# Kernel optimization log

Hardware: AMD Instinct MI355X
Metric: run time of the kernel (lower is better)

## Reference

```python
import jax, jax.numpy as jnp
import numpy as np

N_QUBITS = 4
N_LAYERS = 2
DIM = 2 ** N_QUBITS  # 16
B = 262144


def _cnot_perm(c, t):
    # wire 0 is the most significant bit (pennylane default.qubit convention)
    idx = np.arange(DIM)
    cb = (idx >> (N_QUBITS - 1 - c)) & 1
    return idx ^ (cb << (N_QUBITS - 1 - t))

# all-pairs CNOTs (i, j) for i < j, applied once per layer
CNOT_PERMS = [jnp.asarray(_cnot_perm(i, j)) for i in range(N_QUBITS) for j in range(i + 1, N_QUBITS)]


def _rx(t):
    c = jnp.cos(t / 2).astype(jnp.complex64)
    s = jnp.sin(t / 2).astype(jnp.complex64)
    return jnp.stack([jnp.stack([c, -1j * s], -1), jnp.stack([-1j * s, c], -1)], -2)


def _ry(t):
    c = jnp.cos(t / 2).astype(jnp.complex64)
    s = jnp.sin(t / 2).astype(jnp.complex64)
    return jnp.stack([jnp.stack([c, -s], -1), jnp.stack([s, c], -1)], -2)


def _rz(t):
    e = jnp.exp(-1j * t.astype(jnp.complex64) / 2)
    z = jnp.zeros_like(e)
    return jnp.stack([jnp.stack([e, z], -1), jnp.stack([z, jnp.conj(e)], -1)], -2)


def _apply_1q(state, gate, wire):
    # state: [B, 2,2,2,2]; gate: [2,2] (shared) or [B,2,2] (per-sample)
    ax = 1 + wire
    s = jnp.moveaxis(state, ax, -1)
    if gate.ndim == 2:
        s = jnp.einsum('b...i,ji->b...j', s, gate)
    else:
        s = jnp.einsum('b...i,bji->b...j', s, gate)
    return jnp.moveaxis(s, -1, ax)


def _circuit(x, qw):
    # x: [B, 4] rotation angles; qw: [24] circuit weights. Returns <Z_0>: [B]
    b = x.shape[0]
    state = jnp.zeros((b, DIM), jnp.complex64).at[:, 0].set(1.0)
    state = state.reshape((b,) + (2,) * N_QUBITS)
    for i in range(N_QUBITS):
        state = _apply_1q(state, _rx(x[:, i]), i)
        state = _apply_1q(state, _rz(x[:, i]), i)
    for layer in range(N_LAYERS):
        for i in range(N_QUBITS):
            state = _apply_1q(state, _ry(qw[layer * N_QUBITS + i]), i)
            state = _apply_1q(state, _rz(qw[layer * N_QUBITS + i + N_QUBITS]), i)
        flat = state.reshape(b, DIM)
        for p in CNOT_PERMS:
            flat = flat[:, p]
        state = flat.reshape((b,) + (2,) * N_QUBITS)
        for i in range(N_QUBITS):
            state = _apply_1q(state, _rx(qw[layer * N_QUBITS + i + 2 * N_QUBITS]), i)
    probs = jnp.abs(state.reshape(b, DIM)) ** 2
    zvec = jnp.where(jnp.arange(DIM) < DIM // 2, 1.0, -1.0).astype(probs.dtype)
    return probs @ zvec


def _mlp(q, W1, b1, W2, b2, W3, b3, W4, b4):
    h = jax.nn.relu(q @ W1.T + b1)
    h = jax.nn.relu(h @ W2.T + b2)
    h = jax.nn.relu(h @ W3.T + b3)
    return jax.nn.sigmoid(h @ W4.T + b4)


def setup_inputs() -> dict:
    key = jax.random.key(0)
    ks = jax.random.split(key, 10)
    def lin(k, fo, fi):
        bound = 1.0 / np.sqrt(fi)
        k1, k2 = jax.random.split(k)
        return (jax.random.uniform(k1, (fo, fi), jnp.float32, -bound, bound),
                jax.random.uniform(k2, (fo,), jnp.float32, -bound, bound))
    W1, b1 = lin(ks[2], 32, 1)
    W2, b2 = lin(ks[3], 16, 32)
    W3, b3 = lin(ks[4], 8, 16)
    W4, b4 = lin(ks[5], 1, 8)
    return {
        'x': jax.random.normal(ks[0], (B, N_QUBITS), jnp.float32),
        'qw': jax.random.normal(ks[1], (N_LAYERS * N_QUBITS * 3,), jnp.float32),
        'W1': W1, 'b1': b1, 'W2': W2, 'b2': b2,
        'W3': W3, 'b3': b3, 'W4': W4, 'b4': b4,
    }


def reference(x, qw, W1, b1, W2, b2, W3, b3, W4, b4):
    q = _circuit(x, qw)[:, None]  # [B, 1] quantum expectation values
    return _mlp(q, W1, b1, W2, b2, W3, b3, W4, b4)
```

## Files before the change

### kernel.cpp

```cpp
#include <hip/hip_runtime.h>
#include <math.h>

#define DIM 16

__device__ __forceinline__ void cmul(float ar, float ai, float br, float bi,
                                     float& cr, float& ci) {
  cr = ar * br - ai * bi;
  ci = ar * bi + ai * br;
}

template <int TB>
__device__ __forceinline__ void apply_ryrz(float (&sr)[DIM], float (&si)[DIM],
                                           float cy, float sy, float cz, float sz) {
#pragma unroll
  for (int i = 0; i < DIM; ++i) {
    if (i & TB) continue;
    const int j = i | TB;
    float a0r = sr[i], a0i = si[i], a1r = sr[j], a1i = si[j];
    float t0r = cy * a0r - sy * a1r;
    float t0i = cy * a0i - sy * a1i;
    float t1r = sy * a0r + cy * a1r;
    float t1i = sy * a0i + cy * a1i;
    sr[i] = cz * t0r + sz * t0i;
    si[i] = cz * t0i - sz * t0r;
    sr[j] = cz * t1r - sz * t1i;
    si[j] = cz * t1i + sz * t1r;
  }
}

template <int TB>
__device__ __forceinline__ void apply_rx(float (&sr)[DIM], float (&si)[DIM],
                                         float cx, float sx) {
#pragma unroll
  for (int i = 0; i < DIM; ++i) {
    if (i & TB) continue;
    const int j = i | TB;
    float a0r = sr[i], a0i = si[i], a1r = sr[j], a1i = si[j];
    sr[i] = cx * a0r + sx * a1i;
    si[i] = cx * a0i - sx * a1r;
    sr[j] = cx * a1r + sx * a0i;
    si[j] = cx * a1i - sx * a0r;
  }
}

template <int CB, int TB>
__device__ __forceinline__ void apply_cnot(float (&sr)[DIM], float (&si)[DIM]) {
#pragma unroll
  for (int i = 0; i < DIM; ++i) {
    if (!(i & CB)) continue;
    if (i & TB) continue;
    const int j = i | TB;
    float tr = sr[i], ti = si[i];
    sr[i] = sr[j]; si[i] = si[j];
    sr[j] = tr;    si[j] = ti;
  }
}

__global__ __launch_bounds__(256) void qnn_kernel(
    const float* __restrict__ x, const float* __restrict__ qw,
    const float* __restrict__ W1, const float* __restrict__ b1,
    const float* __restrict__ W2, const float* __restrict__ b2,
    const float* __restrict__ W3, const float* __restrict__ b3,
    const float* __restrict__ W4, const float* __restrict__ b4,
    float* __restrict__ out, int B) {
  int b = blockIdx.x * blockDim.x + threadIdx.x;
  if (b >= B) return;

  float4 xv = reinterpret_cast<const float4*>(x)[b];
  float xs[4] = {xv.x, xv.y, xv.z, xv.w};

  float ur[4][2], ui[4][2];
#pragma unroll
  for (int i = 0; i < 4; ++i) {
    float s, c;
    __sincosf(0.5f * xs[i], &s, &c);
    ur[i][0] = c * c;
    ur[i][1] = s * s;
    ui[i][0] = -c * s;
    ui[i][1] = -c * s;
  }

  float a01r[4], a01i[4], a23r[4], a23i[4];
#pragma unroll
  for (int i0 = 0; i0 < 2; ++i0)
#pragma unroll
    for (int i1 = 0; i1 < 2; ++i1) {
      cmul(ur[0][i0], ui[0][i0], ur[1][i1], ui[1][i1], a01r[i0 * 2 + i1], a01i[i0 * 2 + i1]);
      cmul(ur[2][i0], ui[2][i0], ur[3][i1], ui[3][i1], a23r[i0 * 2 + i1], a23i[i0 * 2 + i1]);
    }
  float sr[DIM], si[DIM];
#pragma unroll
  for (int i = 0; i < DIM; ++i)
    cmul(a01r[i >> 2], a01i[i >> 2], a23r[i & 3], a23i[i & 3], sr[i], si[i]);

#pragma unroll
  for (int layer = 0; layer < 2; ++layer) {
    const int o = layer * 4;

#define RYRZ_W(WIRE, TB)                                                     \
  {                                                                          \
    float sy, cy, sz, cz;                                                    \
    __sincosf(0.5f * qw[o + WIRE], &sy, &cy);                                \
    __sincosf(0.5f * qw[o + WIRE + 4], &sz, &cz);                            \
    apply_ryrz<TB>(sr, si, cy, sy, cz, sz);                                  \
  }
    RYRZ_W(0, 8)
    RYRZ_W(1, 4)
    RYRZ_W(2, 2)
    RYRZ_W(3, 1)
#undef RYRZ_W

    apply_cnot<8, 4>(sr, si);
    apply_cnot<8, 2>(sr, si);
    apply_cnot<8, 1>(sr, si);
    apply_cnot<4, 2>(sr, si);
    apply_cnot<4, 1>(sr, si);
    apply_cnot<2, 1>(sr, si);

#define RX_W(WIRE, TB)                                                       \
  {                                                                          \
    float sx, cx;                                                            \
    __sincosf(0.5f * qw[o + WIRE + 8], &sx, &cx);                            \
    apply_rx<TB>(sr, si, cx, sx);                                            \
  }
    RX_W(0, 8)
    RX_W(1, 4)
    RX_W(2, 2)
    RX_W(3, 1)
#undef RX_W
  }

  float q = 0.f;
#pragma unroll
  for (int i = 0; i < DIM; ++i) {
    float p = fmaf(sr[i], sr[i], si[i] * si[i]);
    q += (i < 8) ? p : -p;
  }

  float h1[32];
#pragma unroll
  for (int j = 0; j < 32; ++j) h1[j] = fmaxf(0.f, fmaf(q, W1[j], b1[j]));

  float h2[16];
#pragma unroll
  for (int k = 0; k < 16; ++k) {
    float acc = b2[k];
#pragma unroll
    for (int j = 0; j < 32; ++j) acc = fmaf(W2[k * 32 + j], h1[j], acc);
    h2[k] = fmaxf(0.f, acc);
  }

  float h3[8];
#pragma unroll
  for (int k = 0; k < 8; ++k) {
    float acc = b3[k];
#pragma unroll
    for (int j = 0; j < 16; ++j) acc = fmaf(W3[k * 16 + j], h2[j], acc);
    h3[k] = fmaxf(0.f, acc);
  }

  float acc = b4[0];
#pragma unroll
  for (int j = 0; j < 8; ++j) acc = fmaf(W4[j], h3[j], acc);

  out[b] = 1.f / (1.f + __expf(-acc));
}

extern "C" void kernel_launch(void* const* d_in, const int* in_sizes, int n_in,
                              void* d_out, int out_size, void* d_ws, size_t ws_size,
                              hipStream_t stream) {
  const float* x  = (const float*)d_in[0];
  const float* qw = (const float*)d_in[1];
  const float* W1 = (const float*)d_in[2];
  const float* b1 = (const float*)d_in[3];
  const float* W2 = (const float*)d_in[4];
  const float* b2 = (const float*)d_in[5];
  const float* W3 = (const float*)d_in[6];
  const float* b3 = (const float*)d_in[7];
  const float* W4 = (const float*)d_in[8];
  const float* b4 = (const float*)d_in[9];
  float* out = (float*)d_out;

  const int B = in_sizes[0] / 4;
  const int block = 256;
  const int grid = (B + block - 1) / block;
  qnn_kernel<<<grid, block, 0, stream>>>(x, qw, W1, b1, W2, b2, W3, b3, W4, b4,
                                         out, B);
}
```

Measured before the change: 89.88 us.

## Fold first-layer rotations into product state and fuse middle gates via setup kernel

Adds a tiny setup kernel that computes the weight-dependent trig values once and writes them to the workspace. Because single-qubit gates commute past nothing but are still local before the first CNOT block, the first layer's Ry/Rz are folded into the per-wire product-state construction. Layer 0's Rx and layer 1's Ry and Rz are merged into one 2x2 unitary per wire. This cuts the number of full 16-amplitude gate sweeps and removes per-thread sincos on uniform weights, at the cost of an extra kernel launch and dense complex 2x2 multiplies.

```diff
diff --git a/kernel.cpp b/kernel.cpp
--- a/kernel.cpp
+++ b/kernel.cpp
@@ -2,6 +2,38 @@
 #include <math.h>
 
 #define DIM 16
+
+__global__ void qnn_setup(const float* __restrict__ qw, float* __restrict__ ws) {
+  int w = threadIdx.x;
+  if (w >= 4) return;
+  float a = qw[0 + w];
+  float b = qw[4 + w];
+  float e0 = qw[8 + w];
+  float c = qw[4 + w];
+  float d = qw[8 + w];
+  float e1 = qw[12 + w];
+
+  ws[w * 4 + 0] = cosf(0.5f * a);
+  ws[w * 4 + 1] = sinf(0.5f * a);
+  ws[w * 4 + 2] = cosf(0.5f * b);
+  ws[w * 4 + 3] = sinf(0.5f * b);
+
+  float cc = cosf(0.5f * c), sc = sinf(0.5f * c);
+  float ce = cosf(0.5f * e0), se = sinf(0.5f * e0);
+  float m00r = cc * ce, m00i =  sc * se;
+  float m01r = -sc * ce, m01i = -cc * se;
+  float m10r =  sc * ce, m10i = -cc * se;
+  float m11r =  cc * ce, m11i = -sc * se;
+  float cd = cosf(0.5f * d), sd = sinf(0.5f * d);
+  float* u = ws + 16 + w * 8;
+  u[0] = cd * m00r + sd * m00i;  u[1] = cd * m00i - sd * m00r;
+  u[2] = cd * m01r + sd * m01i;  u[3] = cd * m01i - sd * m01r;
+  u[4] = cd * m10r - sd * m10i;  u[5] = cd * m10i + sd * m10r;
+  u[6] = cd * m11r - sd * m11i;  u[7] = cd * m11i + sd * m11r;
+
+  ws[48 + w * 2 + 0] = cosf(0.5f * e1);
+  ws[48 + w * 2 + 1] = sinf(0.5f * e1);
+}
 
 __device__ __forceinline__ void cmul(float ar, float ai, float br, float bi,
                                      float& cr, float& ci) {
@@ -10,21 +42,19 @@
 }
 
 template <int TB>
-__device__ __forceinline__ void apply_ryrz(float (&sr)[DIM], float (&si)[DIM],
-                                           float cy, float sy, float cz, float sz) {
+__device__ __forceinline__ void apply_u(float (&sr)[DIM], float (&si)[DIM],
+                                        float u00r, float u00i, float u01r, float u01i,
+                                        float u10r, float u10i, float u11r, float u11i) {
 #pragma unroll
   for (int i = 0; i < DIM; ++i) {
     if (i & TB) continue;
     const int j = i | TB;
-    float a0r = sr[i], a0i = si[i], a1r = sr[j], a1i = si[j];
-    float t0r = cy * a0r - sy * a1r;
-    float t0i = cy * a0i - sy * a1i;
-    float t1r = sy * a0r + cy * a1r;
-    float t1i = sy * a0i + cy * a1i;
-    sr[i] = cz * t0r + sz * t0i;
-    si[i] = cz * t0i - sz * t0r;
-    sr[j] = cz * t1r - sz * t1i;
-    si[j] = cz * t1i + sz * t1r;
+    float ar = sr[i], ai = si[i], br = sr[j], bi = si[j];
+    float nr = u00r * ar - u00i * ai + u01r * br - u01i * bi;
+    float ni = u00r * ai + u00i * ar + u01r * bi + u01i * br;
+    float mr = u10r * ar - u10i * ai + u11r * br - u11i * bi;
+    float mi = u10r * ai + u10i * ar + u11r * bi + u11i * br;
+    sr[i] = nr; si[i] = ni; sr[j] = mr; si[j] = mi;
   }
 }
 
@@ -57,7 +87,7 @@
 }
 
 __global__ __launch_bounds__(256) void qnn_kernel(
-    const float* __restrict__ x, const float* __restrict__ qw,
+    const float* __restrict__ x, const float* __restrict__ ws,
     const float* __restrict__ W1, const float* __restrict__ b1,
     const float* __restrict__ W2, const float* __restrict__ b2,
     const float* __restrict__ W3, const float* __restrict__ b3,
@@ -71,13 +101,17 @@
 
   float ur[4][2], ui[4][2];
 #pragma unroll
-  for (int i = 0; i < 4; ++i) {
+  for (int w = 0; w < 4; ++w) {
     float s, c;
-    __sincosf(0.5f * xs[i], &s, &c);
-    ur[i][0] = c * c;
-    ur[i][1] = s * s;
-    ui[i][0] = -c * s;
-    ui[i][1] = -c * s;
+    __sincosf(0.5f * xs[w], &s, &c);
+    float v0r0 = c * c, v0i0 = -c * s;
+    float v0r1 = s * s, v0i1 = -c * s;
+    float cy = ws[w * 4 + 0], sy = ws[w * 4 + 1];
+    float cz = ws[w * 4 + 2], sz = ws[w * 4 + 3];
+    float t0r = cy * v0r0 - sy * v0r1, t0i = cy * v0i0 - sy * v0i1;
+    float t1r = sy * v0r0 + cy * v0r1, t1i = sy * v0i0 + cy * v0i1;
+    ur[w][0] = cz * t0r + sz * t0i;  ui[w][0] = cz * t0i - sz * t0r;
+    ur[w][1] = cz * t1r - sz * t1i;  ui[w][1] = cz * t1i + sz * t1r;
   }
 
   float a01r[4], a01i[4], a23r[4], a23i[4];
@@ -93,42 +127,35 @@
   for (int i = 0; i < DIM; ++i)
     cmul(a01r[i >> 2], a01i[i >> 2], a23r[i & 3], a23i[i & 3], sr[i], si[i]);
 
-#pragma unroll
-  for (int layer = 0; layer < 2; ++layer) {
-    const int o = layer * 4;
-
-#define RYRZ_W(WIRE, TB)                                                     \
-  {                                                                          \
-    float sy, cy, sz, cz;                                                    \
-    __sincosf(0.5f * qw[o + WIRE], &sy, &cy);                                \
-    __sincosf(0.5f * qw[o + WIRE + 4], &sz, &cz);                            \
-    apply_ryrz<TB>(sr, si, cy, sy, cz, sz);                                  \
-  }
-    RYRZ_W(0, 8)
-    RYRZ_W(1, 4)
-    RYRZ_W(2, 2)
-    RYRZ_W(3, 1)
-#undef RYRZ_W
-
-    apply_cnot<8, 4>(sr, si);
-    apply_cnot<8, 2>(sr, si);
-    apply_cnot<8, 1>(sr, si);
-    apply_cnot<4, 2>(sr, si);
-    apply_cnot<4, 1>(sr, si);
-    apply_cnot<2, 1>(sr, si);
-
-#define RX_W(WIRE, TB)                                                       \
-  {                                                                          \
-    float sx, cx;                                                            \
-    __sincosf(0.5f * qw[o + WIRE + 8], &sx, &cx);                            \
-    apply_rx<TB>(sr, si, cx, sx);                                            \
-  }
-    RX_W(0, 8)
-    RX_W(1, 4)
-    RX_W(2, 2)
-    RX_W(3, 1)
-#undef RX_W
-  }
+  apply_cnot<8, 4>(sr, si);
+  apply_cnot<8, 2>(sr, si);
+  apply_cnot<8, 1>(sr, si);
+  apply_cnot<4, 2>(sr, si);
+  apply_cnot<4, 1>(sr, si);
+  apply_cnot<2, 1>(sr, si);
+
+#define APPLY_U(WIRE, TB)                                                   \
+  apply_u<TB>(sr, si, ws[16 + WIRE * 8 + 0], ws[16 + WIRE * 8 + 1],         \
+              ws[16 + WIRE * 8 + 2], ws[16 + WIRE * 8 + 3],                 \
+              ws[16 + WIRE * 8 + 4], ws[16 + WIRE * 8 + 5],                 \
+              ws[16 + WIRE * 8 + 6], ws[16 + WIRE * 8 + 7]);
+  APPLY_U(0, 8)
+  APPLY_U(1, 4)
+  APPLY_U(2, 2)
+  APPLY_U(3, 1)
+#undef APPLY_U
+
+  apply_cnot<8, 4>(sr, si);
+  apply_cnot<8, 2>(sr, si);
+  apply_cnot<8, 1>(sr, si);
+  apply_cnot<4, 2>(sr, si);
+  apply_cnot<4, 1>(sr, si);
+  apply_cnot<2, 1>(sr, si);
+
+  apply_rx<8>(sr, si, ws[48 + 0], ws[49 + 0]);
+  apply_rx<4>(sr, si, ws[48 + 2], ws[49 + 2]);
+  apply_rx<2>(sr, si, ws[48 + 4], ws[49 + 4]);
+  apply_rx<1>(sr, si, ws[48 + 6], ws[49 + 6]);
 
   float q = 0.f;
 #pragma unroll
@@ -180,10 +207,13 @@
   const float* W4 = (const float*)d_in[8];
   const float* b4 = (const float*)d_in[9];
   float* out = (float*)d_out;
+  float* ws  = (float*)d_ws;
+
+  qnn_setup<<<1, 64, 0, stream>>>(qw, ws);
 
   const int B = in_sizes[0] / 4;
   const int block = 256;
   const int grid = (B + block - 1) / block;
-  qnn_kernel<<<grid, block, 0, stream>>>(x, qw, W1, b1, W2, b2, W3, b3, W4, b4,
+  qnn_kernel<<<grid, block, 0, stream>>>(x, ws, W1, b1, W2, b2, W3, b3, W4, b4,
                                          out, B);
 }
```

New measurement: 89.56 us. Within noise of the previous version (-0.4%).
